# Kernel optimization log

Measured on AMD Instinct MI355X. Metric: run time of the kernel, lower is better.

The kernel has to match this reference:

```python
import jax, jax.numpy as jnp
import numpy as np

D_MODEL = 768
NUM_HEADS = 12
D_HEAD = D_MODEL // NUM_HEADS


def setup_inputs() -> dict:
    key = jax.random.key(0)
    ks = jax.random.split(key, 11)
    B, S = 1, 4096
    s = 1.0 / np.sqrt(D_MODEL)
    inp = {
        'q': jax.random.normal(ks[0], (B, S, D_MODEL), dtype=jnp.float32),
        'k': jax.random.normal(ks[1], (B, S, D_MODEL), dtype=jnp.float32),
        'v': jax.random.normal(ks[2], (B, S, D_MODEL), dtype=jnp.float32),
        'wq': jax.random.normal(ks[3], (D_MODEL, D_MODEL), dtype=jnp.float32) * s,
        'bq': jnp.zeros((D_MODEL,), dtype=jnp.float32),
        'wk': jax.random.normal(ks[4], (D_MODEL, D_MODEL), dtype=jnp.float32) * s,
        'bk': jnp.zeros((D_MODEL,), dtype=jnp.float32),
        'wv': jax.random.normal(ks[5], (D_MODEL, D_MODEL), dtype=jnp.float32) * s,
        'bv': jnp.zeros((D_MODEL,), dtype=jnp.float32),
        'wo': jax.random.normal(ks[6], (D_MODEL, D_MODEL), dtype=jnp.float32) * s,
        'bo': jnp.zeros((D_MODEL,), dtype=jnp.float32),
    }
    return inp


def reference(q, k, v, wq, bq, wk, bk, wv, bv, wo, bo):
    B, S, _ = q.shape
    # linear projections (torch Linear: x @ W^T + b)
    qh = (q @ wq.T + bq).reshape(B, S, NUM_HEADS, D_HEAD).transpose(0, 2, 1, 3)
    kh = (k @ wk.T + bk).reshape(B, S, NUM_HEADS, D_HEAD).transpose(0, 2, 1, 3)
    vh = (v @ wv.T + bv).reshape(B, S, NUM_HEADS, D_HEAD).transpose(0, 2, 1, 3)
    scores = jnp.einsum('bhqd,bhkd->bhqk', qh, kh) / jnp.sqrt(jnp.float32(D_HEAD))
    causal = jnp.tril(jnp.ones((S, S), dtype=bool))  # [S,S] causal mask
    scores = jnp.where(causal, scores, jnp.finfo(scores.dtype).min)
    attn = jax.nn.softmax(scores, axis=-1)  # dropout omitted (eval mode)
    out = jnp.einsum('bhqk,bhkd->bhqd', attn, vh)
    out = out.transpose(0, 2, 1, 3).reshape(B, S, D_MODEL)
    return out @ wo.T + bo
```

## Files before the change

### kernel.cpp

```cpp
#include <hip/hip_runtime.h>
#include <stdint.h>

typedef __attribute__((ext_vector_type(8))) short short8;
typedef __attribute__((ext_vector_type(2))) float float2v;
typedef __attribute__((ext_vector_type(4))) float float4v;
typedef __attribute__((ext_vector_type(16))) float f32x16;
typedef __attribute__((ext_vector_type(2))) uint32_t uint32x2;
typedef __attribute__((ext_vector_type(4))) uint32_t uint32x4;
typedef __attribute__((ext_vector_type(2))) unsigned int uint2v;

__device__ __forceinline__ uint32_t pkbf(float a, float b) {
  uint32_t r;
  asm("v_cvt_pk_bf16_f32 %0, %1, %2" : "=v"(r) : "v"(a), "v"(b));
  return r;
}

__device__ __forceinline__ float2v pkadd(float2v a, float2v b) {
  float2v d;
  asm("v_pk_add_f32 %0, %1, %2" : "=v"(d) : "v"(a), "v"(b));
  return d;
}

__device__ __forceinline__ float fexp2(float x) {
#if __has_builtin(__builtin_amdgcn_exp2f)
  return __builtin_amdgcn_exp2f(x);
#else
  return exp2f(x);
#endif
}

__device__ __forceinline__ uint2v plswap(uint32_t a, uint32_t b) {
#if __has_builtin(__builtin_amdgcn_permlane32_swap)
  return __builtin_amdgcn_permlane32_swap(a, b, false, false);
#else
  asm("v_permlane32_swap_b32 %0, %1" : "+v"(a), "+v"(b));
  uint2v r;
  r[0] = a;
  r[1] = b;
  return r;
#endif
}

__device__ __forceinline__ void gll16(const unsigned short* g, unsigned short* l) {
  __builtin_amdgcn_global_load_lds(
      (const __attribute__((address_space(1))) void*)g,
      (__attribute__((address_space(3))) void*)l, 16, 0, 0);
}

struct CvtArgs {
  const float* src[7];
  unsigned short* dst[7];
};

__global__ __launch_bounds__(256) void cvt_all(CvtArgs a) {
  const int bid = blockIdx.x;
  int t, off;
  if (bid < 4608) { t = bid / 1536; off = bid - t * 1536; }
  else { const int b2 = bid - 4608; t = 3 + b2 / 288; off = b2 - (t - 3) * 288; }
  const size_t i = (size_t)off * 256 + threadIdx.x;
  const float4v* p = (const float4v*)(a.src[t] + i * 8);
  float4v x = p[0], y = p[1];
  uint32x4 o;
  o[0] = pkbf(x[0], x[1]);
  o[1] = pkbf(x[2], x[3]);
  o[2] = pkbf(y[0], y[1]);
  o[3] = pkbf(y[2], y[3]);
  *(uint32x4*)(a.dst[t] + i * 8) = o;
}

__global__ __launch_bounds__(256) void gemm_qkv(
    const unsigned short* __restrict__ xq, const unsigned short* __restrict__ xk,
    const unsigned short* __restrict__ xv,
    const unsigned short* __restrict__ wqb, const unsigned short* __restrict__ wkb,
    const unsigned short* __restrict__ wvb,
    const float* __restrict__ bq, const float* __restrict__ bk,
    const float* __restrict__ bv,
    unsigned short* __restrict__ Qp, unsigned short* __restrict__ Kp,
    unsigned short* __restrict__ Vt, float qscale)
{
  __shared__ unsigned short As[64 * 64];
  __shared__ unsigned short Ws[128 * 64];
  const int z = blockIdx.z;
  const unsigned short* A = z == 0 ? xq : z == 1 ? xk : xv;
  const unsigned short* W = z == 0 ? wqb : z == 1 ? wkb : wvb;
  const float* bias = z == 0 ? bq : z == 1 ? bk : bv;
  const int M = 4096, N = 768, K = 768;
  const int tid = threadIdx.x, wave = tid >> 6, lane = tid & 63;
  const int g = lane >> 4, l16 = lane & 15;
  const int sw = l16 & 7;
  const int m0 = blockIdx.x * 64, n0 = blockIdx.y * 128;
  const int wm = (wave & 1) * 32, wn = (wave >> 1) * 64;
  const int r8 = lane >> 3, skg = lane & 7;

  float4v acc[4][2] = {};

  for (int k0 = 0; k0 < K; k0 += 64) {
    if (k0) __syncthreads();
    #pragma unroll
    for (int cc = 0; cc < 2; ++cc) {
      const int row = wave * 16 + cc * 8 + r8;
      const int kg = skg ^ (row & 7);
      gll16(A + (size_t)(m0 + row) * K + k0 + kg * 8, &As[(wave * 16 + cc * 8) * 64]);
    }
    #pragma unroll
    for (int cc = 0; cc < 4; ++cc) {
      const int row = wave * 32 + cc * 8 + r8;
      const int kg = skg ^ (row & 7);
      gll16(W + (size_t)(n0 + row) * K + k0 + kg * 8, &Ws[(wave * 32 + cc * 8) * 64]);
    }
    __syncthreads();
    #pragma unroll
    for (int kk = 0; kk < 2; ++kk) {
      const int kg = ((kk * 4 + g) ^ sw) * 8;
      short8 xf[2], wf[4];
      #pragma unroll
      for (int t = 0; t < 2; ++t) xf[t] = *(const short8*)&As[(wm + t * 16 + l16) * 64 + kg];
      #pragma unroll
      for (int t = 0; t < 4; ++t) wf[t] = *(const short8*)&Ws[(wn + t * 16 + l16) * 64 + kg];
      if (z < 2) {
        #pragma unroll
        for (int i = 0; i < 4; ++i)
          #pragma unroll
          for (int j = 0; j < 2; ++j)
            acc[i][j] = __builtin_amdgcn_mfma_f32_16x16x32_bf16(wf[i], xf[j], acc[i][j], 0, 0, 0);
      } else {
        #pragma unroll
        for (int b = 0; b < 4; ++b)
          #pragma unroll
          for (int a2 = 0; a2 < 2; ++a2)
            acc[b][a2] = __builtin_amdgcn_mfma_f32_16x16x32_bf16(xf[a2], wf[b], acc[b][a2], 0, 0, 0);
      }
    }
  }

  if (z < 2) {
    unsigned short* O = z == 0 ? Qp : Kp;
    const float osc = z == 0 ? qscale : 1.0f;
    #pragma unroll
    for (int i = 0; i < 4; ++i) {
      const int nb = n0 + wn + i * 16 + 4 * g;
      const float4v bb = *(const float4v*)&bias[nb];
      #pragma unroll
      for (int j = 0; j < 2; ++j) {
        const int m = m0 + wm + j * 16 + l16;
        uint32x2 pk;
        pk[0] = pkbf((acc[i][j][0] + bb[0]) * osc, (acc[i][j][1] + bb[1]) * osc);
        pk[1] = pkbf((acc[i][j][2] + bb[2]) * osc, (acc[i][j][3] + bb[3]) * osc);
        *(uint32x2*)(O + (size_t)m * N + nb) = pk;
      }
    }
  } else {
    #pragma unroll
    for (int b = 0; b < 4; ++b) {
      const int n = n0 + wn + b * 16 + l16;
      const float bb = bias[n];
      #pragma unroll
      for (int a2 = 0; a2 < 2; ++a2) {
        const int mb = m0 + wm + a2 * 16 + 4 * g;
        uint32x2 pk;
        pk[0] = pkbf(acc[b][a2][0] + bb, acc[b][a2][1] + bb);
        pk[1] = pkbf(acc[b][a2][2] + bb, acc[b][a2][3] + bb);
        *(uint32x2*)(Vt + (size_t)n * M + mb) = pk;
      }
    }
  }
}

__global__ __launch_bounds__(256, 4) void flash_part(
    const unsigned short* __restrict__ Qp,
    const unsigned short* __restrict__ Kp,
    const unsigned short* __restrict__ Vt,
    unsigned short* __restrict__ Opart,
    float* __restrict__ lpart)
{
  __shared__ unsigned short lds_k[2][64 * 64];
  __shared__ unsigned short lds_v[2][64 * 64];
  const int S = 4096, DM = 768;

  const int gid = blockIdx.x;
  const int h = gid % 12;
  const int e = 79 - gid / 12;
  int t, c;
  if (e < 8)       { t = e;                c = 0; }
  else if (e < 24) { t = 8 + (e - 8) / 2;  c = (e - 8) % 2; }
  else if (e < 48) { t = 16 + (e - 24) / 3; c = (e - 24) % 3; }
  else             { t = 24 + (e - 48) / 4; c = (e - 48) % 4; }
  const int kb0 = c * 16;
  const int kbe = min(kb0 + 16, 2 * t + 2);

  const int tid = threadIdx.x, wave = tid >> 6, lane = tid & 63;
  const int l31 = lane & 31, hi = lane >> 5, sw7 = lane & 7;
  const int qbase = t * 128 + wave * 32;
  const int qrow = qbase + l31;

  short8 qf[4];
  {
    const unsigned short* qp = Qp + (size_t)qrow * DM + h * 64 + hi * 8;
    qf[0] = *(const short8*)(qp);
    qf[1] = *(const short8*)(qp + 16);
    qf[2] = *(const short8*)(qp + 32);
    qf[3] = *(const short8*)(qp + 48);
  }

  f32x16 o0 = {}, o1 = {};
  float2v lsA = {0.f, 0.f}, lsB = {0.f, 0.f};

  const int strow = wave * 16 + (lane >> 3);
  const int skg = lane & 7;

  #pragma unroll
  for (int cc = 0; cc < 2; ++cc) {
    const int row = strow + cc * 8;
    const int kg = skg ^ (row & 7);
    gll16(Kp + (size_t)(kb0 * 64 + row) * DM + h * 64 + kg * 8,
          &lds_k[0][(wave * 16 + cc * 8) * 64]);
    gll16(Vt + (size_t)(h * 64 + row) * S + kb0 * 64 + kg * 8,
          &lds_v[0][(wave * 16 + cc * 8) * 64]);
  }
  __syncthreads();

  for (int kb = kb0; kb < kbe; ++kb) {
    const int cur = kb & 1;
    if (kb + 1 < kbe) {
      const int nb = cur ^ 1;
      #pragma unroll
      for (int cc = 0; cc < 2; ++cc) {
        const int row = strow + cc * 8;
        const int kg = skg ^ (row & 7);
        gll16(Kp + (size_t)((kb + 1) * 64 + row) * DM + h * 64 + kg * 8,
              &lds_k[nb][(wave * 16 + cc * 8) * 64]);
        gll16(Vt + (size_t)(h * 64 + row) * S + (kb + 1) * 64 + kg * 8,
              &lds_v[nb][(wave * 16 + cc * 8) * 64]);
      }
    }
    const unsigned short* kc = lds_k[cur];
    const unsigned short* vc = lds_v[cur];

    f32x16 s0 = {}, s1 = {};
    __builtin_amdgcn_s_setprio(1);
    #pragma unroll
    for (int d4 = 0; d4 < 4; ++d4) {
      const int cg = ((2 * d4 + hi) ^ sw7) * 8;
      short8 ka = *(const short8*)&kc[l31 * 64 + cg];
      short8 kb2 = *(const short8*)&kc[(32 + l31) * 64 + cg];
      s0 = __builtin_amdgcn_mfma_f32_32x32x16_bf16(ka, qf[d4], s0, 0, 0, 0);
      s1 = __builtin_amdgcn_mfma_f32_32x32x16_bf16(kb2, qf[d4], s1, 0, 0, 0);
    }
    __builtin_amdgcn_s_setprio(0);

    const bool diag = (kb + 1) * 64 > qbase;
    short8 pb[4];
    auto sm_pack = [&](const f32x16& sv, int ks, short8* pbp) {
      #pragma unroll
      for (int jh = 0; jh < 2; ++jh) {
        float pe[8];
        if (diag) {
          #pragma unroll
          for (int rr = 0; rr < 8; ++rr) {
            const int key = kb * 64 + ks + (rr & 3) + 8 * (2 * jh + (rr >> 2)) + 4 * hi;
            pe[rr] = fexp2(key <= qrow ? sv[jh * 8 + rr] : -1e30f);
          }
        } else {
          #pragma unroll
          for (int rr = 0; rr < 8; ++rr) pe[rr] = fexp2(sv[jh * 8 + rr]);
        }
        float2v p01 = {pe[0], pe[1]}, p23 = {pe[2], pe[3]};
        float2v p45 = {pe[4], pe[5]}, p67 = {pe[6], pe[7]};
        lsA = pkadd(lsA, pkadd(p01, p45));
        lsB = pkadd(lsB, pkadd(p23, p67));
        const uint32_t x01 = pkbf(pe[0], pe[1]);
        const uint32_t x23 = pkbf(pe[2], pe[3]);
        const uint32_t y01 = pkbf(pe[4], pe[5]);
        const uint32_t y23 = pkbf(pe[6], pe[7]);
        uint2v r01 = plswap(x01, y01);
        uint2v r23 = plswap(x23, y23);
        union { uint32x4 u; short8 s; } w;
        w.u[0] = r01[0];
        w.u[1] = r23[0];
        w.u[2] = r01[1];
        w.u[3] = r23[1];
        pbp[jh] = w.s;
      }
    };
    sm_pack(s0, 0, &pb[0]);
    sm_pack(s1, 32, &pb[2]);

    __builtin_amdgcn_s_setprio(1);
    #pragma unroll
    for (int kk = 0; kk < 4; ++kk) {
      const int cg = ((2 * kk + hi) ^ sw7) * 8;
      short8 va0 = *(const short8*)&vc[l31 * 64 + cg];
      short8 va1 = *(const short8*)&vc[(32 + l31) * 64 + cg];
      o0 = __builtin_amdgcn_mfma_f32_32x32x16_bf16(va0, pb[kk], o0, 0, 0, 0);
      o1 = __builtin_amdgcn_mfma_f32_32x32x16_bf16(va1, pb[kk], o1, 0, 0, 0);
    }
    __builtin_amdgcn_s_setprio(0);

    __syncthreads();
  }

  float L = (lsA[0] + lsA[1]) + (lsB[0] + lsB[1]);
  L += __shfl_xor(L, 32);
  const int slot = (h * 32 + t) * 4 + c;
  if (hi == 0) lpart[slot * 128 + wave * 32 + l31] = L;
  unsigned short* ob = Opart + (size_t)slot * 8192 + (size_t)(wave * 32 + l31) * 64;
  #pragma unroll
  for (int dt = 0; dt < 2; ++dt) {
    const f32x16& oo = dt ? o1 : o0;
    #pragma unroll
    for (int a = 0; a < 4; ++a) {
      uint32x2 ov;
      ov[0] = pkbf(oo[4 * a + 0], oo[4 * a + 1]);
      ov[1] = pkbf(oo[4 * a + 2], oo[4 * a + 3]);
      *(uint32x2*)(ob + dt * 32 + 8 * a + 4 * hi) = ov;
    }
  }
}

__global__ __launch_bounds__(256) void flash_combine(
    const unsigned short* __restrict__ Opart, const float* __restrict__ lpart,
    unsigned short* __restrict__ AO)
{
  const int t = blockIdx.x, h = blockIdx.y;
  const int nc = (2 * t + 17) >> 4;
  const int slot0 = (h * 32 + t) * 4;
  const int tid = threadIdx.x;
  const int qr = tid >> 2, dc = (tid & 3) * 16;
  #pragma unroll
  for (int it = 0; it < 2; ++it) {
    const int ql = it * 64 + qr;
    float acc[16];
    #pragma unroll
    for (int j = 0; j < 16; ++j) acc[j] = 0.0f;
    float lsum = 0.0f;
    for (int cc = 0; cc < nc; ++cc) {
      const int slot = slot0 + cc;
      lsum += lpart[slot * 128 + ql];
      const uint32x4* p = (const uint32x4*)(Opart + (size_t)slot * 8192 + ql * 64 + dc);
      uint32x4 w0 = p[0], w1 = p[1];
      #pragma unroll
      for (int j = 0; j < 4; ++j) {
        union { uint32_t u; float f; } lo, hi;
        lo.u = w0[j] << 16; hi.u = w0[j] & 0xffff0000u;
        acc[2 * j] += lo.f; acc[2 * j + 1] += hi.f;
        lo.u = w1[j] << 16; hi.u = w1[j] & 0xffff0000u;
        acc[8 + 2 * j] += lo.f; acc[8 + 2 * j + 1] += hi.f;
      }
    }
    const float inv = 1.0f / lsum;
    uint32x4 o0, o1;
    #pragma unroll
    for (int j = 0; j < 4; ++j) {
      o0[j] = pkbf(acc[2 * j] * inv, acc[2 * j + 1] * inv);
      o1[j] = pkbf(acc[8 + 2 * j] * inv, acc[8 + 2 * j + 1] * inv);
    }
    unsigned short* dst = AO + (size_t)(t * 128 + ql) * 768 + h * 64 + dc;
    *(uint32x4*)dst = o0;
    *(uint32x4*)(dst + 8) = o1;
  }
}

__global__ __launch_bounds__(256) void gemm_out(
    const unsigned short* __restrict__ A, const unsigned short* __restrict__ W,
    const float* __restrict__ bias, float* __restrict__ Out)
{
  __shared__ unsigned short As[64 * 64];
  __shared__ unsigned short Ws[64 * 64];
  const int N = 768, K = 768;
  const int tid = threadIdx.x, wave = tid >> 6, lane = tid & 63;
  const int g = lane >> 4, l16 = lane & 15;
  const int sw = l16 & 7;
  const int m0 = blockIdx.x * 64, n0 = blockIdx.y * 64;
  const int wm = (wave & 1) * 32, wn = (wave >> 1) * 32;
  const int r8 = lane >> 3, skg = lane & 7;

  float4v acc[2][2] = {};

  for (int k0 = 0; k0 < K; k0 += 64) {
    if (k0) __syncthreads();
    #pragma unroll
    for (int cc = 0; cc < 2; ++cc) {
      const int row = wave * 16 + cc * 8 + r8;
      const int kg = skg ^ (row & 7);
      gll16(A + (size_t)(m0 + row) * K + k0 + kg * 8, &As[(wave * 16 + cc * 8) * 64]);
    }
    #pragma unroll
    for (int cc = 0; cc < 2; ++cc) {
      const int row = wave * 16 + cc * 8 + r8;
      const int kg = skg ^ (row & 7);
      gll16(W + (size_t)(n0 + row) * K + k0 + kg * 8, &Ws[(wave * 16 + cc * 8) * 64]);
    }
    __syncthreads();
    #pragma unroll
    for (int kk = 0; kk < 2; ++kk) {
      const int kg = ((kk * 4 + g) ^ sw) * 8;
      short8 xf[2], wf[2];
      #pragma unroll
      for (int t = 0; t < 2; ++t) {
        xf[t] = *(const short8*)&As[(wm + t * 16 + l16) * 64 + kg];
        wf[t] = *(const short8*)&Ws[(wn + t * 16 + l16) * 64 + kg];
      }
      #pragma unroll
      for (int i = 0; i < 2; ++i)
        #pragma unroll
        for (int j = 0; j < 2; ++j)
          acc[i][j] = __builtin_amdgcn_mfma_f32_16x16x32_bf16(wf[i], xf[j], acc[i][j], 0, 0, 0);
    }
  }

  #pragma unroll
  for (int i = 0; i < 2; ++i) {
    const int nb = n0 + wn + i * 16 + 4 * g;
    const float4v bb = *(const float4v*)&bias[nb];
    #pragma unroll
    for (int j = 0; j < 2; ++j) {
      const int m = m0 + wm + j * 16 + l16;
      float4v ov;
      #pragma unroll
      for (int rr = 0; rr < 4; ++rr) ov[rr] = acc[i][j][rr] + bb[rr];
      *(float4v*)(Out + (size_t)m * N + nb) = ov;
    }
  }
}

extern "C" void kernel_launch(void* const* d_in, const int* in_sizes, int n_in,
                              void* d_out, int out_size, void* d_ws, size_t ws_size,
                              hipStream_t stream) {
  const float* q  = (const float*)d_in[0];
  const float* k  = (const float*)d_in[1];
  const float* v  = (const float*)d_in[2];
  const float* wq = (const float*)d_in[3];
  const float* bq = (const float*)d_in[4];
  const float* wk = (const float*)d_in[5];
  const float* bk = (const float*)d_in[6];
  const float* wv = (const float*)d_in[7];
  const float* bv = (const float*)d_in[8];
  const float* wo = (const float*)d_in[9];
  const float* bo = (const float*)d_in[10];
  float* out = (float*)d_out;

  const int S = 4096, D = 768;
  unsigned short* Qp    = (unsigned short*)d_ws;
  unsigned short* Kp    = Qp  + (size_t)S * D;
  unsigned short* Vt    = Kp  + (size_t)S * D;
  unsigned short* AO    = Vt  + (size_t)S * D;
  unsigned short* xq    = AO  + (size_t)S * D;
  unsigned short* xk    = xq  + (size_t)S * D;
  unsigned short* xv    = xk  + (size_t)S * D;
  unsigned short* wqb   = xv  + (size_t)S * D;
  unsigned short* wkb   = wqb + (size_t)D * D;
  unsigned short* wvb   = wkb + (size_t)D * D;
  unsigned short* wob   = wvb + (size_t)D * D;
  unsigned short* Opart = wob + (size_t)D * D;
  float*          lpart = (float*)(Opart + (size_t)1536 * 8192);

  CvtArgs ca;
  ca.src[0] = q;  ca.dst[0] = xq;
  ca.src[1] = k;  ca.dst[1] = xk;
  ca.src[2] = v;  ca.dst[2] = xv;
  ca.src[3] = wq; ca.dst[3] = wqb;
  ca.src[4] = wk; ca.dst[4] = wkb;
  ca.src[5] = wv; ca.dst[5] = wvb;
  ca.src[6] = wo; ca.dst[6] = wob;

  const float SC = 0.125f * 1.44269504089f;
  dim3 blk(256);
  cvt_all<<<dim3(5760), blk, 0, stream>>>(ca);
  gemm_qkv<<<dim3(64, 6, 3), blk, 0, stream>>>(xq, xk, xv, wqb, wkb, wvb,
                                               bq, bk, bv, Qp, Kp, Vt, SC);
  flash_part<<<dim3(960), blk, 0, stream>>>(Qp, Kp, Vt, Opart, lpart);
  flash_combine<<<dim3(32, 12), blk, 0, stream>>>(Opart, lpart, AO);
  gemm_out<<<dim3(64, 12), blk, 0, stream>>>(AO, wob, bo, out);
}
```

Before: 191.4 us.

## Software-pipeline QK^T of next block with softmax of current in flash kernel

Restructures the flash attention inner loop so the QK^T MFMAs for the next key block are issued in between the exp/pack steps of the current block's softmax. This lets matrix-core work and VALU exp work overlap. K staging is moved two blocks ahead and V staging one block ahead, using separate buffers. The combine kernel is also split so each block handles 64 query rows instead of 128, doubling its grid for more parallelism. The cost is more live registers for the extra score accumulators, which could reduce occupancy.

Measured after the change: 228.7 us. 1.19x slower.

```diff
diff --git a/kernel.cpp b/kernel.cpp
--- a/kernel.cpp
+++ b/kernel.cpp
@@ -208,82 +208,100 @@
   const int strow = wave * 16 + (lane >> 3);
   const int skg = lane & 7;
 
-  #pragma unroll
-  for (int cc = 0; cc < 2; ++cc) {
-    const int row = strow + cc * 8;
-    const int kg = skg ^ (row & 7);
-    gll16(Kp + (size_t)(kb0 * 64 + row) * DM + h * 64 + kg * 8,
-          &lds_k[0][(wave * 16 + cc * 8) * 64]);
-    gll16(Vt + (size_t)(h * 64 + row) * S + kb0 * 64 + kg * 8,
-          &lds_v[0][(wave * 16 + cc * 8) * 64]);
-  }
+  auto stageK = [&](int buf, int kb) {
+    #pragma unroll
+    for (int cc = 0; cc < 2; ++cc) {
+      const int row = strow + cc * 8;
+      const int kg = skg ^ (row & 7);
+      gll16(Kp + (size_t)(kb * 64 + row) * DM + h * 64 + kg * 8,
+            &lds_k[buf][(wave * 16 + cc * 8) * 64]);
+    }
+  };
+  auto stageV = [&](int buf, int kb) {
+    #pragma unroll
+    for (int cc = 0; cc < 2; ++cc) {
+      const int row = strow + cc * 8;
+      const int kg = skg ^ (row & 7);
+      gll16(Vt + (size_t)(h * 64 + row) * S + kb * 64 + kg * 8,
+            &lds_v[buf][(wave * 16 + cc * 8) * 64]);
+    }
+  };
+
+  stageK(kb0 & 1, kb0);
+  if (kb0 + 1 < kbe) stageK((kb0 + 1) & 1, kb0 + 1);
+  stageV(kb0 & 1, kb0);
   __syncthreads();
 
-  for (int kb = kb0; kb < kbe; ++kb) {
-    const int cur = kb & 1;
-    if (kb + 1 < kbe) {
-      const int nb = cur ^ 1;
-      #pragma unroll
-      for (int cc = 0; cc < 2; ++cc) {
-        const int row = strow + cc * 8;
-        const int kg = skg ^ (row & 7);
-        gll16(Kp + (size_t)((kb + 1) * 64 + row) * DM + h * 64 + kg * 8,
-              &lds_k[nb][(wave * 16 + cc * 8) * 64]);
-        gll16(Vt + (size_t)(h * 64 + row) * S + (kb + 1) * 64 + kg * 8,
-              &lds_v[nb][(wave * 16 + cc * 8) * 64]);
-      }
-    }
-    const unsigned short* kc = lds_k[cur];
-    const unsigned short* vc = lds_v[cur];
-
-    f32x16 s0 = {}, s1 = {};
+  f32x16 sc0 = {}, sc1 = {};
+  {
+    const unsigned short* kc = lds_k[kb0 & 1];
     __builtin_amdgcn_s_setprio(1);
     #pragma unroll
     for (int d4 = 0; d4 < 4; ++d4) {
       const int cg = ((2 * d4 + hi) ^ sw7) * 8;
       short8 ka = *(const short8*)&kc[l31 * 64 + cg];
       short8 kb2 = *(const short8*)&kc[(32 + l31) * 64 + cg];
-      s0 = __builtin_amdgcn_mfma_f32_32x32x16_bf16(ka, qf[d4], s0, 0, 0, 0);
-      s1 = __builtin_amdgcn_mfma_f32_32x32x16_bf16(kb2, qf[d4], s1, 0, 0, 0);
+      sc0 = __builtin_amdgcn_mfma_f32_32x32x16_bf16(ka, qf[d4], sc0, 0, 0, 0);
+      sc1 = __builtin_amdgcn_mfma_f32_32x32x16_bf16(kb2, qf[d4], sc1, 0, 0, 0);
     }
     __builtin_amdgcn_s_setprio(0);
-
+  }
+  __syncthreads();
+
+  for (int kb = kb0; kb < kbe; ++kb) {
+    if (kb + 2 < kbe) stageK(kb & 1, kb + 2);
+    if (kb + 1 < kbe) stageV((kb + 1) & 1, kb + 1);
+
+    const bool nx = kb + 1 < kbe;
+    const unsigned short* kn = lds_k[(kb + 1) & 1];
+    const unsigned short* vc = lds_v[kb & 1];
     const bool diag = (kb + 1) * 64 > qbase;
+
+    auto sm_q = [&](const f32x16& sv, int ks, int jh) -> short8 {
+      float pe[8];
+      if (diag) {
+        #pragma unroll
+        for (int rr = 0; rr < 8; ++rr) {
+          const int key = kb * 64 + ks + (rr & 3) + 8 * (2 * jh + (rr >> 2)) + 4 * hi;
+          pe[rr] = fexp2(key <= qrow ? sv[jh * 8 + rr] : -1e30f);
+        }
+      } else {
+        #pragma unroll
+        for (int rr = 0; rr < 8; ++rr) pe[rr] = fexp2(sv[jh * 8 + rr]);
+      }
+      float2v p01 = {pe[0], pe[1]}, p23 = {pe[2], pe[3]};
+      float2v p45 = {pe[4], pe[5]}, p67 = {pe[6], pe[7]};
+      lsA = pkadd(lsA, pkadd(p01, p45));
+      lsB = pkadd(lsB, pkadd(p23, p67));
+      const uint32_t x01 = pkbf(pe[0], pe[1]);
+      const uint32_t x23 = pkbf(pe[2], pe[3]);
+      const uint32_t y01 = pkbf(pe[4], pe[5]);
+      const uint32_t y23 = pkbf(pe[6], pe[7]);
+      uint2v r01 = plswap(x01, y01);
+      uint2v r23 = plswap(x23, y23);
+      union { uint32x4 u; short8 s; } w;
+      w.u[0] = r01[0];
+      w.u[1] = r23[0];
+      w.u[2] = r01[1];
+      w.u[3] = r23[1];
+      return w.s;
+    };
+
+    f32x16 sn0 = {}, sn1 = {};
     short8 pb[4];
-    auto sm_pack = [&](const f32x16& sv, int ks, short8* pbp) {
-      #pragma unroll
-      for (int jh = 0; jh < 2; ++jh) {
-        float pe[8];
-        if (diag) {
-          #pragma unroll
-          for (int rr = 0; rr < 8; ++rr) {
-            const int key = kb * 64 + ks + (rr & 3) + 8 * (2 * jh + (rr >> 2)) + 4 * hi;
-            pe[rr] = fexp2(key <= qrow ? sv[jh * 8 + rr] : -1e30f);
-          }
-        } else {
-          #pragma unroll
-          for (int rr = 0; rr < 8; ++rr) pe[rr] = fexp2(sv[jh * 8 + rr]);
-        }
-        float2v p01 = {pe[0], pe[1]}, p23 = {pe[2], pe[3]};
-        float2v p45 = {pe[4], pe[5]}, p67 = {pe[6], pe[7]};
-        lsA = pkadd(lsA, pkadd(p01, p45));
-        lsB = pkadd(lsB, pkadd(p23, p67));
-        const uint32_t x01 = pkbf(pe[0], pe[1]);
-        const uint32_t x23 = pkbf(pe[2], pe[3]);
-        const uint32_t y01 = pkbf(pe[4], pe[5]);
-        const uint32_t y23 = pkbf(pe[6], pe[7]);
-        uint2v r01 = plswap(x01, y01);
-        uint2v r23 = plswap(x23, y23);
-        union { uint32x4 u; short8 s; } w;
-        w.u[0] = r01[0];
-        w.u[1] = r23[0];
-        w.u[2] = r01[1];
-        w.u[3] = r23[1];
-        pbp[jh] = w.s;
-      }
-    };
-    sm_pack(s0, 0, &pb[0]);
-    sm_pack(s1, 32, &pb[2]);
+    #pragma unroll
+    for (int d4 = 0; d4 < 4; ++d4) {
+      if (nx) {
+        const int cg = ((2 * d4 + hi) ^ sw7) * 8;
+        short8 ka = *(const short8*)&kn[l31 * 64 + cg];
+        short8 kb2 = *(const short8*)&kn[(32 + l31) * 64 + cg];
+        __builtin_amdgcn_s_setprio(1);
+        sn0 = __builtin_amdgcn_mfma_f32_32x32x16_bf16(ka, qf[d4], sn0, 0, 0, 0);
+        sn1 = __builtin_amdgcn_mfma_f32_32x32x16_bf16(kb2, qf[d4], sn1, 0, 0, 0);
+        __builtin_amdgcn_s_setprio(0);
+      }
+      pb[d4] = (d4 < 2) ? sm_q(sc0, 0, d4) : sm_q(sc1, 32, d4 - 2);
+    }
 
     __builtin_amdgcn_s_setprio(1);
     #pragma unroll
@@ -297,6 +315,8 @@
     __builtin_amdgcn_s_setprio(0);
 
     __syncthreads();
+    sc0 = sn0;
+    sc1 = sn1;
   }
 
   float L = (lsA[0] + lsA[1]) + (lsB[0] + lsB[1]);
@@ -321,43 +341,41 @@
     const unsigned short* __restrict__ Opart, const float* __restrict__ lpart,
     unsigned short* __restrict__ AO)
 {
-  const int t = blockIdx.x, h = blockIdx.y;
+  const int t2 = blockIdx.x, h = blockIdx.y;
+  const int t = t2 >> 1;
   const int nc = (2 * t + 17) >> 4;
   const int slot0 = (h * 32 + t) * 4;
   const int tid = threadIdx.x;
   const int qr = tid >> 2, dc = (tid & 3) * 16;
+  const int ql = (t2 & 1) * 64 + qr;
+  float acc[16];
   #pragma unroll
-  for (int it = 0; it < 2; ++it) {
-    const int ql = it * 64 + qr;
-    float acc[16];
-    #pragma unroll
-    for (int j = 0; j < 16; ++j) acc[j] = 0.0f;
-    float lsum = 0.0f;
-    for (int cc = 0; cc < nc; ++cc) {
-      const int slot = slot0 + cc;
-      lsum += lpart[slot * 128 + ql];
-      const uint32x4* p = (const uint32x4*)(Opart + (size_t)slot * 8192 + ql * 64 + dc);
-      uint32x4 w0 = p[0], w1 = p[1];
-      #pragma unroll
-      for (int j = 0; j < 4; ++j) {
-        union { uint32_t u; float f; } lo, hi;
-        lo.u = w0[j] << 16; hi.u = w0[j] & 0xffff0000u;
-        acc[2 * j] += lo.f; acc[2 * j + 1] += hi.f;
-        lo.u = w1[j] << 16; hi.u = w1[j] & 0xffff0000u;
-        acc[8 + 2 * j] += lo.f; acc[8 + 2 * j + 1] += hi.f;
-      }
-    }
-    const float inv = 1.0f / lsum;
-    uint32x4 o0, o1;
+  for (int j = 0; j < 16; ++j) acc[j] = 0.0f;
+  float lsum = 0.0f;
+  for (int cc = 0; cc < nc; ++cc) {
+    const int slot = slot0 + cc;
+    lsum += lpart[slot * 128 + ql];
+    const uint32x4* p = (const uint32x4*)(Opart + (size_t)slot * 8192 + ql * 64 + dc);
+    uint32x4 w0 = p[0], w1 = p[1];
     #pragma unroll
     for (int j = 0; j < 4; ++j) {
-      o0[j] = pkbf(acc[2 * j] * inv, acc[2 * j + 1] * inv);
-      o1[j] = pkbf(acc[8 + 2 * j] * inv, acc[8 + 2 * j + 1] * inv);
-    }
-    unsigned short* dst = AO + (size_t)(t * 128 + ql) * 768 + h * 64 + dc;
-    *(uint32x4*)dst = o0;
-    *(uint32x4*)(dst + 8) = o1;
-  }
+      union { uint32_t u; float f; } lo, hi;
+      lo.u = w0[j] << 16; hi.u = w0[j] & 0xffff0000u;
+      acc[2 * j] += lo.f; acc[2 * j + 1] += hi.f;
+      lo.u = w1[j] << 16; hi.u = w1[j] & 0xffff0000u;
+      acc[8 + 2 * j] += lo.f; acc[8 + 2 * j + 1] += hi.f;
+    }
+  }
+  const float inv = 1.0f / lsum;
+  uint32x4 o0, o1;
+  #pragma unroll
+  for (int j = 0; j < 4; ++j) {
+    o0[j] = pkbf(acc[2 * j] * inv, acc[2 * j + 1] * inv);
+    o1[j] = pkbf(acc[8 + 2 * j] * inv, acc[8 + 2 * j + 1] * inv);
+  }
+  unsigned short* dst = AO + (size_t)(t * 128 + ql) * 768 + h * 64 + dc;
+  *(uint32x4*)dst = o0;
+  *(uint32x4*)(dst + 8) = o1;
 }
 
 __global__ __launch_bounds__(256) void gemm_out(
@@ -469,6 +487,6 @@
   gemm_qkv<<<dim3(64, 6, 3), blk, 0, stream>>>(xq, xk, xv, wqb, wkb, wvb,
                                                bq, bk, bv, Qp, Kp, Vt, SC);
   flash_part<<<dim3(960), blk, 0, stream>>>(Qp, Kp, Vt, Opart, lpart);
-  flash_combine<<<dim3(32, 12), blk, 0, stream>>>(Opart, lpart, AO);
+  flash_combine<<<dim3(64, 12), blk, 0, stream>>>(Opart, lpart, AO);
   gemm_out<<<dim3(64, 12), blk, 0, stream>>>(AO, wob, bo, out);
 }
```

## Fuse fp32-to-bf16 conversion into GEMM tile loads and split combine blocks

Applied to the files above, without the earlier changes.

Removes the separate conversion kernel: the QKV and output GEMMs now read fp32 inputs and weights directly, convert them to bf16 in registers, and write them into swizzled LDS instead of using direct global-to-LDS loads. This drops one launch plus a full write and reread of bf16 copies of the activations and weights. In exchange, each GEMM reads twice the bytes per tile and loses the async LDS load path, and weights are converted again by every block. The combine kernel is also split so each block handles 64 rows instead of 128, doubling its grid for more parallelism.

After: 195.7 us. 1.02x slower.

```diff
diff --git a/kernel.cpp b/kernel.cpp
--- a/kernel.cpp
+++ b/kernel.cpp
@@ -47,32 +47,22 @@
       (__attribute__((address_space(3))) void*)l, 16, 0, 0);
 }
 
-struct CvtArgs {
-  const float* src[7];
-  unsigned short* dst[7];
-};
-
-__global__ __launch_bounds__(256) void cvt_all(CvtArgs a) {
-  const int bid = blockIdx.x;
-  int t, off;
-  if (bid < 4608) { t = bid / 1536; off = bid - t * 1536; }
-  else { const int b2 = bid - 4608; t = 3 + b2 / 288; off = b2 - (t - 3) * 288; }
-  const size_t i = (size_t)off * 256 + threadIdx.x;
-  const float4v* p = (const float4v*)(a.src[t] + i * 8);
-  float4v x = p[0], y = p[1];
-  uint32x4 o;
-  o[0] = pkbf(x[0], x[1]);
-  o[1] = pkbf(x[2], x[3]);
-  o[2] = pkbf(y[0], y[1]);
-  o[3] = pkbf(y[2], y[3]);
-  *(uint32x4*)(a.dst[t] + i * 8) = o;
+__device__ __forceinline__ void cvt_cell(const float* src, unsigned short* dst) {
+  const float4v a0 = *(const float4v*)src;
+  const float4v a1 = *(const float4v*)(src + 4);
+  uint32x4 w;
+  w[0] = pkbf(a0[0], a0[1]);
+  w[1] = pkbf(a0[2], a0[3]);
+  w[2] = pkbf(a1[0], a1[1]);
+  w[3] = pkbf(a1[2], a1[3]);
+  *(uint32x4*)dst = w;
 }
 
 __global__ __launch_bounds__(256) void gemm_qkv(
-    const unsigned short* __restrict__ xq, const unsigned short* __restrict__ xk,
-    const unsigned short* __restrict__ xv,
-    const unsigned short* __restrict__ wqb, const unsigned short* __restrict__ wkb,
-    const unsigned short* __restrict__ wvb,
+    const float* __restrict__ xq, const float* __restrict__ xk,
+    const float* __restrict__ xv,
+    const float* __restrict__ wq, const float* __restrict__ wk,
+    const float* __restrict__ wv,
     const float* __restrict__ bq, const float* __restrict__ bk,
     const float* __restrict__ bv,
     unsigned short* __restrict__ Qp, unsigned short* __restrict__ Kp,
@@ -81,8 +71,8 @@
   __shared__ unsigned short As[64 * 64];
   __shared__ unsigned short Ws[128 * 64];
   const int z = blockIdx.z;
-  const unsigned short* A = z == 0 ? xq : z == 1 ? xk : xv;
-  const unsigned short* W = z == 0 ? wqb : z == 1 ? wkb : wvb;
+  const float* A = z == 0 ? xq : z == 1 ? xk : xv;
+  const float* W = z == 0 ? wq : z == 1 ? wk : wv;
   const float* bias = z == 0 ? bq : z == 1 ? bk : bv;
   const int M = 4096, N = 768, K = 768;
   const int tid = threadIdx.x, wave = tid >> 6, lane = tid & 63;
@@ -100,13 +90,13 @@
     for (int cc = 0; cc < 2; ++cc) {
       const int row = wave * 16 + cc * 8 + r8;
       const int kg = skg ^ (row & 7);
-      gll16(A + (size_t)(m0 + row) * K + k0 + kg * 8, &As[(wave * 16 + cc * 8) * 64]);
+      cvt_cell(A + (size_t)(m0 + row) * K + k0 + kg * 8, &As[row * 64 + skg * 8]);
     }
     #pragma unroll
     for (int cc = 0; cc < 4; ++cc) {
       const int row = wave * 32 + cc * 8 + r8;
       const int kg = skg ^ (row & 7);
-      gll16(W + (size_t)(n0 + row) * K + k0 + kg * 8, &Ws[(wave * 32 + cc * 8) * 64]);
+      cvt_cell(W + (size_t)(n0 + row) * K + k0 + kg * 8, &Ws[row * 64 + skg * 8]);
     }
     __syncthreads();
     #pragma unroll
@@ -321,47 +311,45 @@
     const unsigned short* __restrict__ Opart, const float* __restrict__ lpart,
     unsigned short* __restrict__ AO)
 {
-  const int t = blockIdx.x, h = blockIdx.y;
+  const int t2 = blockIdx.x, h = blockIdx.y;
+  const int t = t2 >> 1;
   const int nc = (2 * t + 17) >> 4;
   const int slot0 = (h * 32 + t) * 4;
   const int tid = threadIdx.x;
   const int qr = tid >> 2, dc = (tid & 3) * 16;
+  const int ql = (t2 & 1) * 64 + qr;
+  float acc[16];
   #pragma unroll
-  for (int it = 0; it < 2; ++it) {
-    const int ql = it * 64 + qr;
-    float acc[16];
-    #pragma unroll
-    for (int j = 0; j < 16; ++j) acc[j] = 0.0f;
-    float lsum = 0.0f;
-    for (int cc = 0; cc < nc; ++cc) {
-      const int slot = slot0 + cc;
-      lsum += lpart[slot * 128 + ql];
-      const uint32x4* p = (const uint32x4*)(Opart + (size_t)slot * 8192 + ql * 64 + dc);
-      uint32x4 w0 = p[0], w1 = p[1];
-      #pragma unroll
-      for (int j = 0; j < 4; ++j) {
-        union { uint32_t u; float f; } lo, hi;
-        lo.u = w0[j] << 16; hi.u = w0[j] & 0xffff0000u;
-        acc[2 * j] += lo.f; acc[2 * j + 1] += hi.f;
-        lo.u = w1[j] << 16; hi.u = w1[j] & 0xffff0000u;
-        acc[8 + 2 * j] += lo.f; acc[8 + 2 * j + 1] += hi.f;
-      }
-    }
-    const float inv = 1.0f / lsum;
-    uint32x4 o0, o1;
+  for (int j = 0; j < 16; ++j) acc[j] = 0.0f;
+  float lsum = 0.0f;
+  for (int cc = 0; cc < nc; ++cc) {
+    const int slot = slot0 + cc;
+    lsum += lpart[slot * 128 + ql];
+    const uint32x4* p = (const uint32x4*)(Opart + (size_t)slot * 8192 + ql * 64 + dc);
+    uint32x4 w0 = p[0], w1 = p[1];
     #pragma unroll
     for (int j = 0; j < 4; ++j) {
-      o0[j] = pkbf(acc[2 * j] * inv, acc[2 * j + 1] * inv);
-      o1[j] = pkbf(acc[8 + 2 * j] * inv, acc[8 + 2 * j + 1] * inv);
-    }
-    unsigned short* dst = AO + (size_t)(t * 128 + ql) * 768 + h * 64 + dc;
-    *(uint32x4*)dst = o0;
-    *(uint32x4*)(dst + 8) = o1;
-  }
+      union { uint32_t u; float f; } lo, hi;
+      lo.u = w0[j] << 16; hi.u = w0[j] & 0xffff0000u;
+      acc[2 * j] += lo.f; acc[2 * j + 1] += hi.f;
+      lo.u = w1[j] << 16; hi.u = w1[j] & 0xffff0000u;
+      acc[8 + 2 * j] += lo.f; acc[8 + 2 * j + 1] += hi.f;
+    }
+  }
+  const float inv = 1.0f / lsum;
+  uint32x4 o0, o1;
+  #pragma unroll
+  for (int j = 0; j < 4; ++j) {
+    o0[j] = pkbf(acc[2 * j] * inv, acc[2 * j + 1] * inv);
+    o1[j] = pkbf(acc[8 + 2 * j] * inv, acc[8 + 2 * j + 1] * inv);
+  }
+  unsigned short* dst = AO + (size_t)(t * 128 + ql) * 768 + h * 64 + dc;
+  *(uint32x4*)dst = o0;
+  *(uint32x4*)(dst + 8) = o1;
 }
 
 __global__ __launch_bounds__(256) void gemm_out(
-    const unsigned short* __restrict__ A, const unsigned short* __restrict__ W,
+    const unsigned short* __restrict__ A, const float* __restrict__ W,
     const float* __restrict__ bias, float* __restrict__ Out)
 {
   __shared__ unsigned short As[64 * 64];
@@ -388,7 +376,7 @@
     for (int cc = 0; cc < 2; ++cc) {
       const int row = wave * 16 + cc * 8 + r8;
       const int kg = skg ^ (row & 7);
-      gll16(W + (size_t)(n0 + row) * K + k0 + kg * 8, &Ws[(wave * 16 + cc * 8) * 64]);
+      cvt_cell(W + (size_t)(n0 + row) * K + k0 + kg * 8, &Ws[row * 64 + skg * 8]);
     }
     __syncthreads();
     #pragma unroll
@@ -444,31 +432,14 @@
   unsigned short* Kp    = Qp  + (size_t)S * D;
   unsigned short* Vt    = Kp  + (size_t)S * D;
   unsigned short* AO    = Vt  + (size_t)S * D;
-  unsigned short* xq    = AO  + (size_t)S * D;
-  unsigned short* xk    = xq  + (size_t)S * D;
-  unsigned short* xv    = xk  + (size_t)S * D;
-  unsigned short* wqb   = xv  + (size_t)S * D;
-  unsigned short* wkb   = wqb + (size_t)D * D;
-  unsigned short* wvb   = wkb + (size_t)D * D;
-  unsigned short* wob   = wvb + (size_t)D * D;
-  unsigned short* Opart = wob + (size_t)D * D;
+  unsigned short* Opart = AO  + (size_t)S * D;
   float*          lpart = (float*)(Opart + (size_t)1536 * 8192);
-
-  CvtArgs ca;
-  ca.src[0] = q;  ca.dst[0] = xq;
-  ca.src[1] = k;  ca.dst[1] = xk;
-  ca.src[2] = v;  ca.dst[2] = xv;
-  ca.src[3] = wq; ca.dst[3] = wqb;
-  ca.src[4] = wk; ca.dst[4] = wkb;
-  ca.src[5] = wv; ca.dst[5] = wvb;
-  ca.src[6] = wo; ca.dst[6] = wob;
 
   const float SC = 0.125f * 1.44269504089f;
   dim3 blk(256);
-  cvt_all<<<dim3(5760), blk, 0, stream>>>(ca);
-  gemm_qkv<<<dim3(64, 6, 3), blk, 0, stream>>>(xq, xk, xv, wqb, wkb, wvb,
+  gemm_qkv<<<dim3(64, 6, 3), blk, 0, stream>>>(q, k, v, wq, wk, wv,
                                                bq, bk, bv, Qp, Kp, Vt, SC);
   flash_part<<<dim3(960), blk, 0, stream>>>(Qp, Kp, Vt, Opart, lpart);
-  flash_combine<<<dim3(32, 12), blk, 0, stream>>>(Opart, lpart, AO);
-  gemm_out<<<dim3(64, 12), blk, 0, stream>>>(AO, wob, bo, out);
-}
+  flash_combine<<<dim3(64, 12), blk, 0, stream>>>(Opart, lpart, AO);
+  gemm_out<<<dim3(64, 12), blk, 0, stream>>>(AO, wo, bo, out);
+}
```

## Fuse flash split-KV combine into output projection GEMM A-tile loading

Applied to the files above, without the earlier changes.

Removes the separate flash_combine kernel and the AO intermediate buffer. gemm_out now reads the partial bf16 outputs and row sums directly, reduces and normalizes them in registers, and writes the A tile into shared memory itself. The next k-slice of partials is loaded into registers while the MFMAs run, giving software prefetch. The cost is that each of the 12 N-column blocks redoes the combine reduction for the same rows, and the loop now has an extra barrier per iteration.

Result: slower. 201.4 us (+5.2%).

```diff
diff --git a/kernel.cpp b/kernel.cpp
--- a/kernel.cpp
+++ b/kernel.cpp
@@ -317,52 +317,10 @@
   }
 }
 
-__global__ __launch_bounds__(256) void flash_combine(
+__global__ __launch_bounds__(256) void gemm_out(
     const unsigned short* __restrict__ Opart, const float* __restrict__ lpart,
-    unsigned short* __restrict__ AO)
-{
-  const int t = blockIdx.x, h = blockIdx.y;
-  const int nc = (2 * t + 17) >> 4;
-  const int slot0 = (h * 32 + t) * 4;
-  const int tid = threadIdx.x;
-  const int qr = tid >> 2, dc = (tid & 3) * 16;
-  #pragma unroll
-  for (int it = 0; it < 2; ++it) {
-    const int ql = it * 64 + qr;
-    float acc[16];
-    #pragma unroll
-    for (int j = 0; j < 16; ++j) acc[j] = 0.0f;
-    float lsum = 0.0f;
-    for (int cc = 0; cc < nc; ++cc) {
-      const int slot = slot0 + cc;
-      lsum += lpart[slot * 128 + ql];
-      const uint32x4* p = (const uint32x4*)(Opart + (size_t)slot * 8192 + ql * 64 + dc);
-      uint32x4 w0 = p[0], w1 = p[1];
-      #pragma unroll
-      for (int j = 0; j < 4; ++j) {
-        union { uint32_t u; float f; } lo, hi;
-        lo.u = w0[j] << 16; hi.u = w0[j] & 0xffff0000u;
-        acc[2 * j] += lo.f; acc[2 * j + 1] += hi.f;
-        lo.u = w1[j] << 16; hi.u = w1[j] & 0xffff0000u;
-        acc[8 + 2 * j] += lo.f; acc[8 + 2 * j + 1] += hi.f;
-      }
-    }
-    const float inv = 1.0f / lsum;
-    uint32x4 o0, o1;
-    #pragma unroll
-    for (int j = 0; j < 4; ++j) {
-      o0[j] = pkbf(acc[2 * j] * inv, acc[2 * j + 1] * inv);
-      o1[j] = pkbf(acc[8 + 2 * j] * inv, acc[8 + 2 * j + 1] * inv);
-    }
-    unsigned short* dst = AO + (size_t)(t * 128 + ql) * 768 + h * 64 + dc;
-    *(uint32x4*)dst = o0;
-    *(uint32x4*)(dst + 8) = o1;
-  }
-}
-
-__global__ __launch_bounds__(256) void gemm_out(
-    const unsigned short* __restrict__ A, const unsigned short* __restrict__ W,
-    const float* __restrict__ bias, float* __restrict__ Out)
+    const unsigned short* __restrict__ W, const float* __restrict__ bias,
+    float* __restrict__ Out)
 {
   __shared__ unsigned short As[64 * 64];
   __shared__ unsigned short Ws[64 * 64];
@@ -374,37 +332,95 @@
   const int wm = (wave & 1) * 32, wn = (wave >> 1) * 32;
   const int r8 = lane >> 3, skg = lane & 7;
 
+  const int t = m0 >> 7;
+  const int ql0 = m0 & 127;
+  const int nc = (2 * t + 17) >> 4;
+  const int slot0 = t * 4;
+
+  int srow[2], skgx[2];
+  #pragma unroll
+  for (int cc = 0; cc < 2; ++cc) {
+    srow[cc] = wave * 16 + cc * 8 + r8;
+    skgx[cc] = skg ^ (srow[cc] & 7);
+  }
+
+  uint32x4 rv[2][4];
+  float lpv[2][4];
+  auto loadA = [&](int h) {
+    const int sb = h * 128 + slot0;
+    #pragma unroll
+    for (int cc = 0; cc < 2; ++cc) {
+      const size_t ro = (size_t)(ql0 + srow[cc]) * 64 + skgx[cc] * 8;
+      #pragma unroll
+      for (int c = 0; c < 4; ++c)
+        if (c < nc) {
+          rv[cc][c] = *(const uint32x4*)(Opart + (size_t)(sb + c) * 8192 + ro);
+          lpv[cc][c] = lpart[(sb + c) * 128 + ql0 + srow[cc]];
+        }
+    }
+  };
+  auto writeA = [&]() {
+    #pragma unroll
+    for (int cc = 0; cc < 2; ++cc) {
+      float a8[8] = {0.f, 0.f, 0.f, 0.f, 0.f, 0.f, 0.f, 0.f};
+      float L = 0.f;
+      #pragma unroll
+      for (int c = 0; c < 4; ++c)
+        if (c < nc) {
+          L += lpv[cc][c];
+          #pragma unroll
+          for (int j = 0; j < 4; ++j) {
+            union { uint32_t u; float f; } lo, hi;
+            lo.u = rv[cc][c][j] << 16;
+            hi.u = rv[cc][c][j] & 0xffff0000u;
+            a8[2 * j] += lo.f;
+            a8[2 * j + 1] += hi.f;
+          }
+        }
+      const float inv = 1.0f / L;
+      uint32x4 w;
+      #pragma unroll
+      for (int j = 0; j < 4; ++j) w[j] = pkbf(a8[2 * j] * inv, a8[2 * j + 1] * inv);
+      *(uint32x4*)&As[srow[cc] * 64 + skg * 8] = w;
+    }
+  };
+  auto dmaW = [&](int k0) {
+    #pragma unroll
+    for (int cc = 0; cc < 2; ++cc)
+      gll16(W + (size_t)(n0 + srow[cc]) * K + k0 + skgx[cc] * 8,
+            &Ws[(wave * 16 + cc * 8) * 64]);
+  };
+
   float4v acc[2][2] = {};
 
+  loadA(0);
+  dmaW(0);
+  writeA();
+  __syncthreads();
+
   for (int k0 = 0; k0 < K; k0 += 64) {
-    if (k0) __syncthreads();
-    #pragma unroll
-    for (int cc = 0; cc < 2; ++cc) {
-      const int row = wave * 16 + cc * 8 + r8;
-      const int kg = skg ^ (row & 7);
-      gll16(A + (size_t)(m0 + row) * K + k0 + kg * 8, &As[(wave * 16 + cc * 8) * 64]);
-    }
-    #pragma unroll
-    for (int cc = 0; cc < 2; ++cc) {
-      const int row = wave * 16 + cc * 8 + r8;
-      const int kg = skg ^ (row & 7);
-      gll16(W + (size_t)(n0 + row) * K + k0 + kg * 8, &Ws[(wave * 16 + cc * 8) * 64]);
-    }
-    __syncthreads();
+    const bool more = (k0 + 64 < K);
+    if (more) loadA((k0 >> 6) + 1);
     #pragma unroll
     for (int kk = 0; kk < 2; ++kk) {
       const int kg = ((kk * 4 + g) ^ sw) * 8;
       short8 xf[2], wf[2];
       #pragma unroll
-      for (int t = 0; t < 2; ++t) {
-        xf[t] = *(const short8*)&As[(wm + t * 16 + l16) * 64 + kg];
-        wf[t] = *(const short8*)&Ws[(wn + t * 16 + l16) * 64 + kg];
+      for (int tt = 0; tt < 2; ++tt) {
+        xf[tt] = *(const short8*)&As[(wm + tt * 16 + l16) * 64 + kg];
+        wf[tt] = *(const short8*)&Ws[(wn + tt * 16 + l16) * 64 + kg];
       }
       #pragma unroll
       for (int i = 0; i < 2; ++i)
         #pragma unroll
         for (int j = 0; j < 2; ++j)
           acc[i][j] = __builtin_amdgcn_mfma_f32_16x16x32_bf16(wf[i], xf[j], acc[i][j], 0, 0, 0);
+    }
+    if (more) {
+      __syncthreads();
+      dmaW(k0 + 64);
+      writeA();
+      __syncthreads();
     }
   }
 
@@ -443,8 +459,7 @@
   unsigned short* Qp    = (unsigned short*)d_ws;
   unsigned short* Kp    = Qp  + (size_t)S * D;
   unsigned short* Vt    = Kp  + (size_t)S * D;
-  unsigned short* AO    = Vt  + (size_t)S * D;
-  unsigned short* xq    = AO  + (size_t)S * D;
+  unsigned short* xq    = Vt  + (size_t)S * D;
   unsigned short* xk    = xq  + (size_t)S * D;
   unsigned short* xv    = xk  + (size_t)S * D;
   unsigned short* wqb   = xv  + (size_t)S * D;
@@ -469,6 +484,5 @@
   gemm_qkv<<<dim3(64, 6, 3), blk, 0, stream>>>(xq, xk, xv, wqb, wkb, wvb,
                                                bq, bk, bv, Qp, Kp, Vt, SC);
   flash_part<<<dim3(960), blk, 0, stream>>>(Qp, Kp, Vt, Opart, lpart);
-  flash_combine<<<dim3(32, 12), blk, 0, stream>>>(Opart, lpart, AO);
-  gemm_out<<<dim3(64, 12), blk, 0, stream>>>(AO, wob, bo, out);
-}
+  gemm_out<<<dim3(64, 12), blk, 0, stream>>>(Opart, lpart, wob, bo, out);
+}
```
